# Kernel optimization log

Measured on AMD Instinct MI355X. Metric: run time of the kernel, lower is better.

## Reference

```python
import jax, jax.numpy as jnp
import numpy as np

# Model dims (see init_kwargs)
B, S, H = 1, 1024, 2048
NH, NKV, HD = 16, 4, 128       # query heads, kv heads (GQA), head dim
RD = 64                        # partial rotary dim
E, TOPK, I = 8, 2, 1024        # experts, top-k, expert intermediate
EPS = 1e-6
THETA = 1000000.0


def setup_inputs() -> dict:
    key = jax.random.key(0)
    ks = jax.random.split(key, 12)
    s = 0.02  # init scale
    return {
        "hidden_states": jax.random.normal(ks[0], (B, S, H), jnp.float32),
        "position_ids": jnp.tile(jnp.arange(S, dtype=jnp.int32), (B, 1)),
        "ln1_w": jnp.ones((H,), jnp.float32),
        "q_norm_w": jnp.ones((NH * HD,), jnp.float32),
        "k_norm_w": jnp.ones((NKV * HD,), jnp.float32),
        "wq": jax.random.normal(ks[1], (H, NH * HD), jnp.float32) * s,
        "wk": jax.random.normal(ks[2], (H, NKV * HD), jnp.float32) * s,
        "wv": jax.random.normal(ks[3], (H, NKV * HD), jnp.float32) * s,
        "wo": jax.random.normal(ks[4], (NH * HD, H), jnp.float32) * s,
        "ln2_w": jnp.ones((H,), jnp.float32),
        "router_w": jax.random.normal(ks[5], (H, E), jnp.float32) * s,
        "router_bias": jax.random.normal(ks[6], (E,), jnp.float32) * 0.1,
        "w_gate": jax.random.normal(ks[7], (E, H, I), jnp.float32) * s,
        "w_up": jax.random.normal(ks[8], (E, H, I), jnp.float32) * s,
        "w_down": jax.random.normal(ks[9], (E, I, H), jnp.float32) * s,
    }


def rmsnorm(x, w):
    # fp32 RMSNorm over full last dim (matches DistributedRMSNorm with tp=1)
    xf = x.astype(jnp.float32)
    r = jax.lax.rsqrt(jnp.mean(xf * xf, axis=-1, keepdims=True) + EPS)
    return (xf * r * w).astype(x.dtype)


def _rope(x, cos, sin):
    # partial rotary: only first RD dims of each head are rotated
    xr, xp = x[..., :RD], x[..., RD:]
    half = RD // 2
    rot = jnp.concatenate([-xr[..., half:], xr[..., :half]], axis=-1)
    return jnp.concatenate([xr * cos + rot * sin, xp], axis=-1)


def reference(hidden_states, position_ids, ln1_w, q_norm_w, k_norm_w,
              wq, wk, wv, wo, ln2_w, router_w, router_bias,
              w_gate, w_up, w_down):
    x = hidden_states
    # --- attention block ---
    h = rmsnorm(x, ln1_w)
    Q = h @ wq  # [B,S,NH*HD]
    K = h @ wk  # [B,S,NKV*HD]
    V = h @ wv
    # MiniMax M2 qk_norm: RMSNorm over FULL projection output BEFORE head reshape
    Q = rmsnorm(Q, q_norm_w)
    K = rmsnorm(K, k_norm_w)
    q = Q.reshape(B, S, NH, HD).transpose(0, 2, 1, 3)   # [B,NH,S,HD]
    k = K.reshape(B, S, NKV, HD).transpose(0, 2, 1, 3)  # [B,NKV,S,HD]
    v = V.reshape(B, S, NKV, HD).transpose(0, 2, 1, 3)
    # partial RoPE
    inv = 1.0 / (THETA ** (jnp.arange(0, RD, 2, dtype=jnp.float32) / RD))
    ang = position_ids.astype(jnp.float32)[:, :, None] * inv  # [B,S,RD/2]
    cos = jnp.concatenate([jnp.cos(ang)] * 2, axis=-1)[:, None]  # [B,1,S,RD]
    sin = jnp.concatenate([jnp.sin(ang)] * 2, axis=-1)[:, None]
    q = _rope(q, cos, sin)
    k = _rope(k, cos, sin)
    # GQA expand
    rep = NH // NKV
    k = jnp.repeat(k, rep, axis=1)
    v = jnp.repeat(v, rep, axis=1)
    scores = jnp.einsum('bhqd,bhkd->bhqk', q, k).astype(jnp.float32) / np.sqrt(HD).astype(np.float32)
    causal = jnp.tril(jnp.ones((S, S), bool))
    scores = jnp.where(causal, scores, jnp.float32(-1e30))
    attn = jax.nn.softmax(scores, axis=-1).astype(v.dtype)
    ctx = jnp.einsum('bhqk,bhkd->bhqd', attn, v)
    attn_out = ctx.transpose(0, 2, 1, 3).reshape(B, S, NH * HD) @ wo
    res = x + attn_out
    # --- MoE block ---
    h2 = rmsnorm(res, ln2_w)
    t = h2.reshape(B * S, H)
    logits = t.astype(jnp.float32) @ router_w        # [T,E]
    sc = jax.nn.sigmoid(logits)
    # top-k chosen on bias-corrected scores; weights from uncorrected scores
    _, ti = jax.lax.top_k(sc + router_bias, TOPK)    # [T,TOPK]
    aff = jnp.take_along_axis(sc, ti, axis=-1)
    aff = aff / jnp.sum(aff, axis=-1, keepdims=True)  # normalize_top_k_affinities
    T = B * S
    combine = jnp.zeros((T, E), jnp.float32).at[jnp.arange(T)[:, None], ti].add(aff)
    # SwiGLU experts (dense-compute, sparse-combine reference for blockwise grouped GEMM)
    g = jnp.einsum('th,ehi->tei', t, w_gate)
    u = jnp.einsum('th,ehi->tei', t, w_up)
    act = jax.nn.silu(g) * u
    eo = jnp.einsum('tei,eih->teh', act, w_down)
    moe = jnp.einsum('te,teh->th', combine.astype(eo.dtype), eo)
    return res + moe.reshape(B, S, H)
```

## Files before the change

kernel.cpp:

```cpp
#include <hip/hip_runtime.h>
#include <hip/hip_bf16.h>
#include <cstdint>

static constexpr int S   = 1024;
static constexpr int H   = 2048;
static constexpr int NH  = 16;
static constexpr int NKV = 4;
static constexpr int HD  = 128;
static constexpr int EXPN = 8;
static constexpr int FFI = 1024;

typedef __bf16 bf16x8 __attribute__((ext_vector_type(8)));
typedef float  f32x4  __attribute__((ext_vector_type(4)));
typedef unsigned short ushortx8 __attribute__((ext_vector_type(8)));
typedef unsigned short ushortx4 __attribute__((ext_vector_type(4)));

#define DEVI __device__ __forceinline__

DEVI unsigned short f2bf(float f) {
    union { float f; uint32_t u; } v; v.f = f;
    uint32_t r = (v.u + 0x7FFFu + ((v.u >> 16) & 1u)) >> 16;
    return (unsigned short)r;
}
DEVI float bf2f(unsigned short s) {
    union { uint32_t u; float f; } v; v.u = ((uint32_t)s) << 16; return v.f;
}

DEVI void atomAdd(float* p, float v) { unsafeAtomicAdd(p, v); }

DEVI void gll16(const unsigned short* g, unsigned short* l) {
    __builtin_amdgcn_global_load_lds(
        (const __attribute__((address_space(1))) unsigned int*)(g),
        (__attribute__((address_space(3))) unsigned int*)(l),
        16, 0, 0);
}

template<int N> DEVI void waitvm() {
    if constexpr (N == 0)      asm volatile("s_waitcnt vmcnt(0)" ::: "memory");
    else if constexpr (N == 2) asm volatile("s_waitcnt vmcnt(2)" ::: "memory");
    else if constexpr (N == 4) asm volatile("s_waitcnt vmcnt(4)" ::: "memory");
    else if constexpr (N == 6) asm volatile("s_waitcnt vmcnt(6)" ::: "memory");
    else static_assert(N == 0 || N == 2 || N == 4 || N == 6, "unsupported vmcnt");
}
DEVI void pipe_barrier() {
    __builtin_amdgcn_sched_barrier(0);
    __builtin_amdgcn_s_barrier();
    __builtin_amdgcn_sched_barrier(0);
}

__global__ __launch_bounds__(256) void transT(const float* __restrict__ in,
                                              unsigned short* __restrict__ outp,
                                              int R, int C)
{
    __shared__ unsigned short tl[64][72];
    int zb = blockIdx.z;
    in   += (size_t)zb * R * C;
    outp += (size_t)zb * R * C;
    int c0 = blockIdx.x * 64, r0 = blockIdx.y * 64;
    int t = threadIdx.x;
    int cq = (t & 15) * 4;
    int rr = t >> 4;
    #pragma unroll
    for (int p = 0; p < 4; ++p) {
        int row = rr + p * 16;
        float4 v = *(const float4*)&in[(size_t)(r0 + row) * C + c0 + cq];
        tl[cq + 0][row] = f2bf(v.x);
        tl[cq + 1][row] = f2bf(v.y);
        tl[cq + 2][row] = f2bf(v.z);
        tl[cq + 3][row] = f2bf(v.w);
    }
    __syncthreads();
    int r8 = (t & 7) * 8;
    int cc = t >> 3;
    #pragma unroll
    for (int p = 0; p < 2; ++p) {
        int col = cc + p * 32;
        ushortx8 v = *(const ushortx8*)&tl[col][r8];
        *(ushortx8*)&outp[(size_t)(c0 + col) * R + r0 + r8] = v;
    }
}

enum { CFG_PROJ3 = 0, CFG_WO = 1, CFG_SCORES = 2, CFG_PV = 3, CFG_GATEUP = 4, CFG_DOWN = 5 };

template<int CFG, int WM, int NI, bool PIPE>
__global__ __launch_bounds__(256, 2) void gemm_k(
    const unsigned short* __restrict__ A,
    const unsigned short* __restrict__ B0,
    const unsigned short* __restrict__ B1,
    const unsigned short* __restrict__ B2,
    float* __restrict__ C0,
    float* __restrict__ C1,
    float* __restrict__ C2,
    unsigned short* __restrict__ Cb,
    const float* __restrict__ X,
    const int* __restrict__ cnt,
    const int* __restrict__ tokList,
    int arg0)
{
    constexpr bool DUAL = (CFG == CFG_GATEUP);
    constexpr int BM = WM * 32;
    constexpr int BN = NI * 32;
    constexpr int ASZ = BM * 64;
    constexpr int BSZ = BN * 64;
    constexpr int NBUF = PIPE ? 3 : 2;
    constexpr int LD = WM + NI + (DUAL ? NI : 0);

    const int tid = threadIdx.x;
    const int m0 = blockIdx.y * BM;
    int n0 = blockIdx.x * BN;

    int M = S;
    int kbeg = 0, kend = 0, LDA = 0, LDBK = 0, LDC = 0;
    const unsigned short* Ap = A;
    const unsigned short* Bb = B0;
    const unsigned short* Bb2 = B1;
    const int* tlist = nullptr;
    float* Cout = C0;
    int head = 0, e = 0, hl = 0;

    if constexpr (CFG == CFG_PROJ3) {
        int xt = blockIdx.x;
        if (xt < 32)      { Bb = B0; Cout = C0; LDC = 2048; n0 = xt * 64; }
        else if (xt < 40) { Bb = B1; Cout = C1; LDC = 512;  n0 = (xt - 32) * 64; }
        else              { Bb = B2; Cout = C2; LDC = 512;  n0 = (xt - 40) * 64; }
        LDA = H; LDBK = H; kend = H;
    } else if constexpr (CFG == CFG_WO) {
        LDA = H; LDBK = H; LDC = H; kend = H;
    } else if constexpr (CFG == CFG_SCORES) {
        hl = blockIdx.z; head = arg0 + hl;
        if (n0 >= m0 + BM) return;
        Ap = A + (size_t)head * S * HD;
        Bb = B0 + (size_t)(head >> 2) * S * HD;
        kend = HD; LDA = HD; LDBK = HD;
    } else if constexpr (CFG == CFG_PV) {
        int z = blockIdx.z; hl = z >> 2; int ks = z & 3;
        head = arg0 + hl;
        int kcap = m0 + BM;
        kbeg = ks * 256;
        if (kbeg >= kcap) return;
        kend = (kbeg + 256 < kcap) ? kbeg + 256 : kcap;
        Ap = A + (size_t)hl * S * S;
        Bb = B0 + (size_t)(head >> 2) * HD * S;
        LDA = S; LDBK = S;
    } else if constexpr (CFG == CFG_GATEUP) {
        e = blockIdx.z;
        M = cnt[e]; if (m0 >= M) return;
        tlist = tokList + e * S;
        Bb  = B0 + (size_t)e * FFI * H;
        Bb2 = B1 + (size_t)e * FFI * H;
        kend = H; LDA = H; LDBK = H;
    } else {
        e = blockIdx.z;
        M = cnt[e]; if (m0 >= M) return;
        Ap = A + (size_t)e * S * FFI;
        Bb = B0 + (size_t)e * H * FFI;
        kend = FFI; LDA = FFI; LDBK = FFI;
    }

    __shared__ unsigned short As[NBUF * ASZ];
    __shared__ unsigned short Bs[NBUF * BSZ];
    __shared__ unsigned short Bs2[DUAL ? NBUF * BSZ : 8];

    const int lane = tid & 63, grp = lane >> 4, r16 = lane & 15;
    const int wid = tid >> 6, wr = wid >> 1, wc = wid & 1;
    const int wbase8 = (tid & 0xFFC0) * 8;

    size_t aoff[WM];
    #pragma unroll
    for (int c = 0; c < WM; ++c) {
        int chunk = c * 256 + tid;
        int row = chunk >> 3;
        int kcs = (chunk & 7) * 8;
        int grow = m0 + row;
        if constexpr (CFG == CFG_GATEUP) { int r2 = grow < M ? grow : M - 1; grow = tlist[r2]; }
        else if constexpr (CFG == CFG_DOWN) { grow = grow < M ? grow : M - 1; }
        aoff[c] = (size_t)grow * LDA + (kcs ^ ((row & 7) << 3));
    }
    size_t boff[NI];
    #pragma unroll
    for (int c = 0; c < NI; ++c) {
        int chunk = c * 256 + tid;
        int row = chunk >> 3;
        int kcs = (chunk & 7) * 8;
        boff[c] = (size_t)(n0 + row) * LDBK + (kcs ^ ((row & 7) << 3));
    }

    auto STAGE = [&](int buf, int k0) {
        #pragma unroll
        for (int c = 0; c < WM; ++c)
            gll16(Ap + aoff[c] + k0, &As[buf * ASZ + c * 2048 + wbase8]);
        #pragma unroll
        for (int c = 0; c < NI; ++c)
            gll16(Bb + boff[c] + k0, &Bs[buf * BSZ + c * 2048 + wbase8]);
        if constexpr (DUAL) {
            #pragma unroll
            for (int c = 0; c < NI; ++c)
                gll16(Bb2 + boff[c] + k0, &Bs2[buf * BSZ + c * 2048 + wbase8]);
        }
    };

    f32x4 acc[WM][NI] = {};
    f32x4 acc2[DUAL ? WM : 1][DUAL ? NI : 1] = {};

    auto COMPUTE = [&](int buf) {
        #pragma unroll
        for (int kk = 0; kk < 64; kk += 32) {
            bf16x8 af[WM], bfr[NI], bfr2[DUAL ? NI : 1];
            #pragma unroll
            for (int mi = 0; mi < WM; ++mi) {
                int r = wr * (WM * 16) + mi * 16 + r16;
                int idx = buf * ASZ + r * 64 + ((kk + grp * 8) ^ ((r & 7) << 3));
                af[mi] = __builtin_bit_cast(bf16x8, *(const ushortx8*)&As[idx]);
            }
            #pragma unroll
            for (int ni = 0; ni < NI; ++ni) {
                int r = wc * (NI * 16) + ni * 16 + r16;
                int idx = buf * BSZ + r * 64 + ((kk + grp * 8) ^ ((r & 7) << 3));
                bfr[ni] = __builtin_bit_cast(bf16x8, *(const ushortx8*)&Bs[idx]);
                if constexpr (DUAL)
                    bfr2[ni] = __builtin_bit_cast(bf16x8, *(const ushortx8*)&Bs2[idx]);
            }
            #pragma unroll
            for (int mi = 0; mi < WM; ++mi)
                #pragma unroll
                for (int ni = 0; ni < NI; ++ni) {
                    acc[mi][ni] = __builtin_amdgcn_mfma_f32_16x16x32_bf16(af[mi], bfr[ni], acc[mi][ni], 0, 0, 0);
                    if constexpr (DUAL)
                        acc2[mi][ni] = __builtin_amdgcn_mfma_f32_16x16x32_bf16(af[mi], bfr2[ni], acc2[mi][ni], 0, 0, 0);
                }
        }
    };

    if constexpr (PIPE) {
        const int nk = (kend - kbeg) >> 6;
        STAGE(0, kbeg);
        if (nk > 1) STAGE(1, kbeg + 64);
        if (nk > 1) waitvm<LD>(); else waitvm<0>();
        pipe_barrier();
        int cur = 0, stg = 2;
        for (int i = 0; i < nk; ++i) {
            if (i + 2 < nk) {
                STAGE(stg, kbeg + (i + 2) * 64);
                stg = (stg == 2) ? 0 : stg + 1;
            }
            COMPUTE(cur);
            cur = (cur == 2) ? 0 : cur + 1;
            if (i + 1 < nk) {
                if (i + 2 < nk) waitvm<LD>();
                else            waitvm<0>();
                pipe_barrier();
            }
        }
    } else {
        int cur = 0;
        STAGE(0, kbeg);
        __syncthreads();
        for (int k0 = kbeg; k0 < kend; k0 += 64) {
            if (k0 + 64 < kend) STAGE(cur ^ 1, k0 + 64);
            COMPUTE(cur);
            __syncthreads();
            cur ^= 1;
        }
    }

    #pragma unroll
    for (int mi = 0; mi < WM; ++mi) {
        #pragma unroll
        for (int ni = 0; ni < NI; ++ni) {
            f32x4 v = acc[mi][ni];
            int col = n0 + wc * (NI * 16) + ni * 16 + r16;
            #pragma unroll
            for (int j = 0; j < 4; ++j) {
                int row = m0 + wr * (WM * 16) + mi * 16 + grp * 4 + j;
                float val = v[j];
                if constexpr (CFG == CFG_PROJ3) {
                    Cout[(size_t)row * LDC + col] = val;
                } else if constexpr (CFG == CFG_WO) {
                    C0[(size_t)row * H + col] = val + X[(size_t)row * H + col];
                } else if constexpr (CFG == CFG_SCORES) {
                    float sv = val * 0.08838834764831845f;
                    if (col > row) sv = -1e30f;
                    Cb[((size_t)hl * S + row) * S + col] = f2bf(sv);
                } else if constexpr (CFG == CFG_PV) {
                    atomAdd(&C0[(size_t)row * 2048 + head * HD + col], val);
                } else if constexpr (CFG == CFG_GATEUP) {
                    if (row < M) {
                        float g = val, u = acc2[mi][ni][j];
                        float a = g / (1.f + expf(-g)) * u;
                        Cb[((size_t)e * S + row) * FFI + col] = f2bf(a);
                    }
                } else {
                    if (row < M) {
                        Cb[((size_t)e * S + row) * H + col] = f2bf(val);
                    }
                }
            }
        }
    }
}

__global__ __launch_bounds__(256) void rms_h(const float* __restrict__ x,
                                             const float* __restrict__ w,
                                             unsigned short* __restrict__ out)
{
    int row = blockIdx.x, tid = threadIdx.x;
    const float* xr = x + (size_t)row * H;
    float4 a = *(const float4*)&xr[tid * 8];
    float4 b = *(const float4*)&xr[tid * 8 + 4];
    float vals[8] = { a.x, a.y, a.z, a.w, b.x, b.y, b.z, b.w };
    float ss = 0;
    #pragma unroll
    for (int j = 0; j < 8; ++j) ss += vals[j] * vals[j];
    __shared__ float red[4];
    #pragma unroll
    for (int o = 32; o; o >>= 1) ss += __shfl_down(ss, o);
    if ((tid & 63) == 0) red[tid >> 6] = ss;
    __syncthreads();
    float tot = red[0] + red[1] + red[2] + red[3];
    float r = rsqrtf(tot * (1.f / H) + 1e-6f);
    ushortx8 ov;
    #pragma unroll
    for (int j = 0; j < 8; ++j) ov[j] = f2bf(vals[j] * r * w[tid * 8 + j]);
    *(ushortx8*)&out[(size_t)row * H + tid * 8] = ov;
}

__global__ __launch_bounds__(256) void qnorm_rope(const float* __restrict__ qbuf,
                                                  const float* __restrict__ qw,
                                                  const int* __restrict__ pos,
                                                  unsigned short* __restrict__ qatt)
{
    int tok = blockIdx.x, tid = threadIdx.x;
    __shared__ float sh[2048];
    __shared__ float red[4];
    const float* xr = qbuf + (size_t)tok * 2048;
    float4 a = *(const float4*)&xr[tid * 8];
    float4 b = *(const float4*)&xr[tid * 8 + 4];
    *(float4*)&sh[tid * 8] = a;
    *(float4*)&sh[tid * 8 + 4] = b;
    float ss = a.x*a.x + a.y*a.y + a.z*a.z + a.w*a.w + b.x*b.x + b.y*b.y + b.z*b.z + b.w*b.w;
    #pragma unroll
    for (int o = 32; o; o >>= 1) ss += __shfl_down(ss, o);
    if ((tid & 63) == 0) red[tid >> 6] = ss;
    __syncthreads();
    float tot = red[0] + red[1] + red[2] + red[3];
    float r = rsqrtf(tot * (1.f / 2048.f) + 1e-6f);
    float p = (float)pos[tok];
    #pragma unroll
    for (int j = 0; j < 8; ++j) {
        int idx = tid * 8 + j;
        int d = idx & 127, hh = idx >> 7;
        float v = sh[idx] * r * qw[idx];
        float o;
        if (d < 64) {
            int jj = d & 31;
            float ang = p * expf((float)jj * -0.43173470268f);
            float c = cosf(ang), sn = sinf(ang);
            if (d < 32) { float v2 = sh[idx + 32] * r * qw[idx + 32]; o = v * c - v2 * sn; }
            else        { float v2 = sh[idx - 32] * r * qw[idx - 32]; o = v * c + v2 * sn; }
        } else o = v;
        qatt[((size_t)hh * S + tok) * HD + d] = f2bf(o);
    }
}

__global__ __launch_bounds__(256) void knorm_rope(const float* __restrict__ kbuf,
                                                  const float* __restrict__ kw,
                                                  const int* __restrict__ pos,
                                                  unsigned short* __restrict__ katt)
{
    int tok = blockIdx.x, tid = threadIdx.x;
    __shared__ float sh[512];
    __shared__ float red[4];
    const float* xr = kbuf + (size_t)tok * 512;
    float2 a = *(const float2*)&xr[tid * 2];
    sh[tid * 2] = a.x; sh[tid * 2 + 1] = a.y;
    float ss = a.x * a.x + a.y * a.y;
    #pragma unroll
    for (int o = 32; o; o >>= 1) ss += __shfl_down(ss, o);
    if ((tid & 63) == 0) red[tid >> 6] = ss;
    __syncthreads();
    float tot = red[0] + red[1] + red[2] + red[3];
    float r = rsqrtf(tot * (1.f / 512.f) + 1e-6f);
    float p = (float)pos[tok];
    #pragma unroll
    for (int j = 0; j < 2; ++j) {
        int idx = tid * 2 + j;
        int d = idx & 127, hh = idx >> 7;
        float v = sh[idx] * r * kw[idx];
        float o;
        if (d < 64) {
            int jj = d & 31;
            float ang = p * expf((float)jj * -0.43173470268f);
            float c = cosf(ang), sn = sinf(ang);
            if (d < 32) { float v2 = sh[idx + 32] * r * kw[idx + 32]; o = v * c - v2 * sn; }
            else        { float v2 = sh[idx - 32] * r * kw[idx - 32]; o = v * c + v2 * sn; }
        } else o = v;
        katt[((size_t)hh * S + tok) * HD + d] = f2bf(o);
    }
}

__global__ __launch_bounds__(256) void softmax_k(unsigned short* __restrict__ sc)
{
    int bid = blockIdx.x;
    int hl = bid >> 10, q = bid & 1023;
    unsigned short* srow = sc + ((size_t)hl * S + q) * S;
    int L = q + 1, tid = threadIdx.x;
    __shared__ float red[4];
    ushortx4 in4 = *(const ushortx4*)&srow[tid * 4];
    float v[4]; float mx = -3.4e38f;
    #pragma unroll
    for (int i = 0; i < 4; ++i) {
        int j = tid * 4 + i;
        if (j < L) { v[i] = bf2f(in4[i]); mx = fmaxf(mx, v[i]); }
        else v[i] = -3.4e38f;
    }
    float m = mx;
    #pragma unroll
    for (int o = 32; o; o >>= 1) m = fmaxf(m, __shfl_down(m, o));
    if ((tid & 63) == 0) red[tid >> 6] = m;
    __syncthreads();
    float M_ = fmaxf(fmaxf(red[0], red[1]), fmaxf(red[2], red[3]));
    __syncthreads();
    float e[4]; float sum = 0;
    #pragma unroll
    for (int i = 0; i < 4; ++i) {
        int j = tid * 4 + i;
        if (j < L) { e[i] = expf(v[i] - M_); sum += e[i]; } else e[i] = 0.f;
    }
    #pragma unroll
    for (int o = 32; o; o >>= 1) sum += __shfl_down(sum, o);
    if ((tid & 63) == 0) red[tid >> 6] = sum;
    __syncthreads();
    float inv = 1.f / (red[0] + red[1] + red[2] + red[3]);
    ushortx4 o4;
    #pragma unroll
    for (int i = 0; i < 4; ++i) o4[i] = f2bf(e[i] * inv);
    *(ushortx4*)&srow[tid * 4] = o4;
}

__global__ void zero_cnt(int* cnt) { if (threadIdx.x < EXPN) cnt[threadIdx.x] = 0; }

__global__ void zerok(float4* __restrict__ p, int n4)
{
    int i = blockIdx.x * 256 + threadIdx.x;
    if (i < n4) p[i] = float4{0.f, 0.f, 0.f, 0.f};
}

__global__ void cvt_k(const float* __restrict__ src, unsigned short* __restrict__ dst)
{
    int i = blockIdx.x * 256 + threadIdx.x;
    float4 a = *(const float4*)&src[i * 8];
    float4 b = *(const float4*)&src[i * 8 + 4];
    float v[8] = { a.x, a.y, a.z, a.w, b.x, b.y, b.z, b.w };
    ushortx8 o;
    #pragma unroll
    for (int j = 0; j < 8; ++j) o[j] = f2bf(v[j]);
    *(ushortx8*)&dst[i * 8] = o;
}

__global__ __launch_bounds__(256) void router_k(const float* __restrict__ res,
                                                const float* __restrict__ ln2w,
                                                const float* __restrict__ rw,
                                                const float* __restrict__ rbias,
                                                int* __restrict__ cnt,
                                                int* __restrict__ tokList,
                                                int* __restrict__ slot,
                                                float* __restrict__ slotw)
{
    int tok = blockIdx.x, tid = threadIdx.x;
    const float* xr = res + (size_t)tok * H;
    float4 a = *(const float4*)&xr[tid * 8];
    float4 b = *(const float4*)&xr[tid * 8 + 4];
    float vals[8] = { a.x, a.y, a.z, a.w, b.x, b.y, b.z, b.w };
    float ss = 0;
    #pragma unroll
    for (int j = 0; j < 8; ++j) ss += vals[j] * vals[j];
    __shared__ float red[4];
    float t_ = ss;
    #pragma unroll
    for (int o = 32; o; o >>= 1) t_ += __shfl_down(t_, o);
    if ((tid & 63) == 0) red[tid >> 6] = t_;
    __syncthreads();
    float tot = red[0] + red[1] + red[2] + red[3];
    float r = rsqrtf(tot * (1.f / H) + 1e-6f);

    float acc[EXPN] = {};
    #pragma unroll
    for (int j = 0; j < 8; ++j) {
        float tv = vals[j] * r * ln2w[tid * 8 + j];
        const float* rp = rw + (size_t)(tid * 8 + j) * EXPN;
        #pragma unroll
        for (int e = 0; e < EXPN; ++e) acc[e] += tv * rp[e];
    }
    __shared__ float r8[4][EXPN];
    #pragma unroll
    for (int e = 0; e < EXPN; ++e) {
        float s_ = acc[e];
        #pragma unroll
        for (int o = 32; o; o >>= 1) s_ += __shfl_down(s_, o);
        acc[e] = s_;
    }
    if ((tid & 63) == 0)
        for (int e = 0; e < EXPN; ++e) r8[tid >> 6][e] = acc[e];
    __syncthreads();
    if (tid == 0) {
        float sg[EXPN];
        for (int e = 0; e < EXPN; ++e) {
            float lg = r8[0][e] + r8[1][e] + r8[2][e] + r8[3][e];
            sg[e] = 1.f / (1.f + expf(-lg));
        }
        int i0 = 0; float b0 = -1e30f;
        for (int e = 0; e < EXPN; ++e) {
            float s_ = sg[e] + rbias[e];
            if (s_ > b0) { b0 = s_; i0 = e; }
        }
        int i1 = -1; float b1 = -1e30f;
        for (int e = 0; e < EXPN; ++e) {
            if (e == i0) continue;
            float s_ = sg[e] + rbias[e];
            if (s_ > b1) { b1 = s_; i1 = e; }
        }
        float a0 = sg[i0], a1 = sg[i1], inv = 1.f / (a0 + a1);
        int p0 = atomicAdd(&cnt[i0], 1);
        tokList[i0 * S + p0] = tok;
        int p1 = atomicAdd(&cnt[i1], 1);
        tokList[i1 * S + p1] = tok;
        slot[tok * 2]     = i0 * S + p0;  slotw[tok * 2]     = a0 * inv;
        slot[tok * 2 + 1] = i1 * S + p1;  slotw[tok * 2 + 1] = a1 * inv;
    }
}

__global__ __launch_bounds__(256) void combine_k(const unsigned short* __restrict__ eo,
                                                 const int* __restrict__ slot,
                                                 const float* __restrict__ slotw,
                                                 float* __restrict__ out)
{
    int t = blockIdx.x;
    int c = threadIdx.x * 8;
    int s0 = slot[t * 2], s1 = slot[t * 2 + 1];
    float w0 = slotw[t * 2], w1 = slotw[t * 2 + 1];
    ushortx8 a = *(const ushortx8*)&eo[(size_t)s0 * H + c];
    ushortx8 b = *(const ushortx8*)&eo[(size_t)s1 * H + c];
    size_t base = (size_t)t * H + c;
    float4 o0 = *(float4*)&out[base];
    float4 o1 = *(float4*)&out[base + 4];
    float ov[8] = { o0.x, o0.y, o0.z, o0.w, o1.x, o1.y, o1.z, o1.w };
    #pragma unroll
    for (int j = 0; j < 8; ++j)
        ov[j] += w0 * bf2f(a[j]) + w1 * bf2f(b[j]);
    *(float4*)&out[base]     = float4{ ov[0], ov[1], ov[2], ov[3] };
    *(float4*)&out[base + 4] = float4{ ov[4], ov[5], ov[6], ov[7] };
}

extern "C" void kernel_launch(void* const* d_in, const int* in_sizes, int n_in,
                              void* d_out, int out_size, void* d_ws, size_t ws_size,
                              hipStream_t stream)
{
    const float* x     = (const float*)d_in[0];
    const int*   pos   = (const int*)d_in[1];
    const float* ln1w  = (const float*)d_in[2];
    const float* qnw   = (const float*)d_in[3];
    const float* knw   = (const float*)d_in[4];
    const float* wq    = (const float*)d_in[5];
    const float* wk    = (const float*)d_in[6];
    const float* wv    = (const float*)d_in[7];
    const float* wo    = (const float*)d_in[8];
    const float* ln2w  = (const float*)d_in[9];
    const float* rw    = (const float*)d_in[10];
    const float* rbias = (const float*)d_in[11];
    const float* wg    = (const float*)d_in[12];
    const float* wu    = (const float*)d_in[13];
    const float* wd    = (const float*)d_in[14];
    float* out = (float*)d_out;

    char* ws = (char*)d_ws;
    const size_t MB = 1024 * 1024;
    unsigned short* h_bf = (unsigned short*)(ws + 0);
    float* qbuf  = (float*)(ws + 4 * MB);
    float* ctxf  = (float*)(ws + 4 * MB);
    float* kbuf  = (float*)(ws + 12 * MB);
    float* vbuf  = (float*)(ws + 14 * MB);
    unsigned short* qatt = (unsigned short*)(ws + 16 * MB);
    unsigned short* katt = (unsigned short*)(ws + 20 * MB);
    unsigned short* vT   = (unsigned short*)(ws + 21 * MB);
    unsigned short* ctx  = (unsigned short*)(ws + 22 * MB);
    unsigned short* tbf  = (unsigned short*)(ws + 26 * MB);
    int*   cnt     = (int*)(ws + 30 * MB);
    int*   tokList = (int*)(ws + 30 * MB + 4096);
    int*   slot    = (int*)(ws + 30 * MB + 512 * 1024);
    float* slotw   = (float*)(ws + 30 * MB + 768 * 1024);
    unsigned short* scores = (unsigned short*)(ws + 31 * MB);
    unsigned short* act = (unsigned short*)(ws + 31 * MB);
    unsigned short* eo  = (unsigned short*)(ws + 47 * MB);
    unsigned short* wqT = (unsigned short*)(ws + 79 * MB);
    unsigned short* wkT = (unsigned short*)(ws + 87 * MB);
    unsigned short* wvT = (unsigned short*)(ws + 89 * MB);
    unsigned short* woT = (unsigned short*)(ws + 91 * MB);
    unsigned short* wgT = (unsigned short*)(ws + 99 * MB);
    unsigned short* wuT = (unsigned short*)(ws + 131 * MB);
    unsigned short* wdT = (unsigned short*)(ws + 163 * MB);

    transT<<<dim3(32, 32, 1), 256, 0, stream>>>(wq, wqT, 2048, 2048);
    transT<<<dim3(8,  32, 1), 256, 0, stream>>>(wk, wkT, 2048, 512);
    transT<<<dim3(8,  32, 1), 256, 0, stream>>>(wv, wvT, 2048, 512);
    transT<<<dim3(32, 32, 1), 256, 0, stream>>>(wo, woT, 2048, 2048);
    transT<<<dim3(16, 32, 8), 256, 0, stream>>>(wg, wgT, 2048, 1024);
    transT<<<dim3(16, 32, 8), 256, 0, stream>>>(wu, wuT, 2048, 1024);
    transT<<<dim3(32, 16, 8), 256, 0, stream>>>(wd, wdT, 1024, 2048);

    rms_h<<<S, 256, 0, stream>>>(x, ln1w, h_bf);

    gemm_k<CFG_PROJ3, 2, 2, true><<<dim3(48, 16, 1), 256, 0, stream>>>(h_bf, wqT, wkT, wvT, qbuf, kbuf, vbuf, nullptr, nullptr, nullptr, nullptr, 0);

    qnorm_rope<<<S, 256, 0, stream>>>(qbuf, qnw, pos, qatt);
    knorm_rope<<<S, 256, 0, stream>>>(kbuf, knw, pos, katt);
    transT<<<dim3(8, 16, 1), 256, 0, stream>>>(vbuf, vT, 1024, 512);
    zerok<<<2048, 256, 0, stream>>>((float4*)ctxf, (8 * MB) / 16);

    gemm_k<CFG_SCORES, 2, 4, false><<<dim3(8, 16, 16), 256, 0, stream>>>(qatt, katt, nullptr, nullptr, nullptr, nullptr, nullptr, scores, nullptr, nullptr, nullptr, 0);
    softmax_k<<<16 * S, 256, 0, stream>>>(scores);
    gemm_k<CFG_PV, 2, 2, true><<<dim3(2, 16, 64), 256, 0, stream>>>(scores, vT, nullptr, nullptr, ctxf, nullptr, nullptr, nullptr, nullptr, nullptr, nullptr, 0);
    cvt_k<<<(S * 2048) / (256 * 8), 256, 0, stream>>>(ctxf, ctx);

    gemm_k<CFG_WO, 2, 2, true><<<dim3(32, 16, 1), 256, 0, stream>>>(ctx, woT, nullptr, nullptr, out, nullptr, nullptr, nullptr, x, nullptr, nullptr, 0);

    rms_h<<<S, 256, 0, stream>>>(out, ln2w, tbf);
    zero_cnt<<<1, 64, 0, stream>>>(cnt);
    router_k<<<S, 256, 0, stream>>>(out, ln2w, rw, rbias, cnt, tokList, slot, slotw);

    gemm_k<CFG_GATEUP, 2, 1, true><<<dim3(32, 16, EXPN), 256, 0, stream>>>(tbf, wgT, wuT, nullptr, nullptr, nullptr, nullptr, act, nullptr, cnt, tokList, 0);
    gemm_k<CFG_DOWN, 2, 2, true><<<dim3(32, 16, EXPN), 256, 0, stream>>>(act, wdT, nullptr, nullptr, nullptr, nullptr, nullptr, eo, nullptr, cnt, tokList, 0);
    combine_k<<<S, 256, 0, stream>>>(eo, slot, slotw, out);
}
```

Before: 352.1 us.

## Concatenate gate/up weights into one GEMM and split SiLU into separate kernel

Measured after the change: 358.4 us. No clear change (+1.8%).

```diff
diff --git a/kernel.cpp b/kernel.cpp
--- a/kernel.cpp
+++ b/kernel.cpp
@@ -50,12 +50,13 @@
 
 __global__ __launch_bounds__(256) void transT(const float* __restrict__ in,
                                               unsigned short* __restrict__ outp,
-                                              int R, int C)
+                                              int R, int C,
+                                              size_t izs, size_t ozs)
 {
     __shared__ unsigned short tl[64][72];
     int zb = blockIdx.z;
-    in   += (size_t)zb * R * C;
-    outp += (size_t)zb * R * C;
+    in   += (size_t)zb * izs;
+    outp += (size_t)zb * ozs;
     int c0 = blockIdx.x * 64, r0 = blockIdx.y * 64;
     int t = threadIdx.x;
     int cq = (t & 15) * 4;
@@ -80,7 +81,7 @@
     }
 }
 
-enum { CFG_PROJ3 = 0, CFG_WO = 1, CFG_SCORES = 2, CFG_PV = 3, CFG_GATEUP = 4, CFG_DOWN = 5 };
+enum { CFG_PROJ3 = 0, CFG_WO = 1, CFG_SCORES = 2, CFG_PV = 3, CFG_GU = 4, CFG_DOWN = 5 };
 
 template<int CFG, int WM, int NI, bool PIPE>
 __global__ __launch_bounds__(256, 2) void gemm_k(
@@ -97,13 +98,12 @@
     const int* __restrict__ tokList,
     int arg0)
 {
-    constexpr bool DUAL = (CFG == CFG_GATEUP);
     constexpr int BM = WM * 32;
     constexpr int BN = NI * 32;
     constexpr int ASZ = BM * 64;
     constexpr int BSZ = BN * 64;
     constexpr int NBUF = PIPE ? 3 : 2;
-    constexpr int LD = WM + NI + (DUAL ? NI : 0);
+    constexpr int LD = WM + NI;
 
     const int tid = threadIdx.x;
     const int m0 = blockIdx.y * BM;
@@ -113,7 +113,6 @@
     int kbeg = 0, kend = 0, LDA = 0, LDBK = 0, LDC = 0;
     const unsigned short* Ap = A;
     const unsigned short* Bb = B0;
-    const unsigned short* Bb2 = B1;
     const int* tlist = nullptr;
     float* Cout = C0;
     int head = 0, e = 0, hl = 0;
@@ -142,12 +141,11 @@
         Ap = A + (size_t)hl * S * S;
         Bb = B0 + (size_t)(head >> 2) * HD * S;
         LDA = S; LDBK = S;
-    } else if constexpr (CFG == CFG_GATEUP) {
+    } else if constexpr (CFG == CFG_GU) {
         e = blockIdx.z;
         M = cnt[e]; if (m0 >= M) return;
         tlist = tokList + e * S;
-        Bb  = B0 + (size_t)e * FFI * H;
-        Bb2 = B1 + (size_t)e * FFI * H;
+        Bb = B0 + (size_t)e * 2048 * H;
         kend = H; LDA = H; LDBK = H;
     } else {
         e = blockIdx.z;
@@ -159,7 +157,6 @@
 
     __shared__ unsigned short As[NBUF * ASZ];
     __shared__ unsigned short Bs[NBUF * BSZ];
-    __shared__ unsigned short Bs2[DUAL ? NBUF * BSZ : 8];
 
     const int lane = tid & 63, grp = lane >> 4, r16 = lane & 15;
     const int wid = tid >> 6, wr = wid >> 1, wc = wid & 1;
@@ -172,7 +169,7 @@
         int row = chunk >> 3;
         int kcs = (chunk & 7) * 8;
         int grow = m0 + row;
-        if constexpr (CFG == CFG_GATEUP) { int r2 = grow < M ? grow : M - 1; grow = tlist[r2]; }
+        if constexpr (CFG == CFG_GU) { int r2 = grow < M ? grow : M - 1; grow = tlist[r2]; }
         else if constexpr (CFG == CFG_DOWN) { grow = grow < M ? grow : M - 1; }
         aoff[c] = (size_t)grow * LDA + (kcs ^ ((row & 7) << 3));
     }
@@ -192,20 +189,14 @@
         #pragma unroll
         for (int c = 0; c < NI; ++c)
             gll16(Bb + boff[c] + k0, &Bs[buf * BSZ + c * 2048 + wbase8]);
-        if constexpr (DUAL) {
-            #pragma unroll
-            for (int c = 0; c < NI; ++c)
-                gll16(Bb2 + boff[c] + k0, &Bs2[buf * BSZ + c * 2048 + wbase8]);
-        }
     };
 
     f32x4 acc[WM][NI] = {};
-    f32x4 acc2[DUAL ? WM : 1][DUAL ? NI : 1] = {};
 
     auto COMPUTE = [&](int buf) {
         #pragma unroll
         for (int kk = 0; kk < 64; kk += 32) {
-            bf16x8 af[WM], bfr[NI], bfr2[DUAL ? NI : 1];
+            bf16x8 af[WM], bfr[NI];
             #pragma unroll
             for (int mi = 0; mi < WM; ++mi) {
                 int r = wr * (WM * 16) + mi * 16 + r16;
@@ -217,17 +208,12 @@
                 int r = wc * (NI * 16) + ni * 16 + r16;
                 int idx = buf * BSZ + r * 64 + ((kk + grp * 8) ^ ((r & 7) << 3));
                 bfr[ni] = __builtin_bit_cast(bf16x8, *(const ushortx8*)&Bs[idx]);
-                if constexpr (DUAL)
-                    bfr2[ni] = __builtin_bit_cast(bf16x8, *(const ushortx8*)&Bs2[idx]);
             }
             #pragma unroll
             for (int mi = 0; mi < WM; ++mi)
                 #pragma unroll
-                for (int ni = 0; ni < NI; ++ni) {
+                for (int ni = 0; ni < NI; ++ni)
                     acc[mi][ni] = __builtin_amdgcn_mfma_f32_16x16x32_bf16(af[mi], bfr[ni], acc[mi][ni], 0, 0, 0);
-                    if constexpr (DUAL)
-                        acc2[mi][ni] = __builtin_amdgcn_mfma_f32_16x16x32_bf16(af[mi], bfr2[ni], acc2[mi][ni], 0, 0, 0);
-                }
         }
     };
 
@@ -283,11 +269,9 @@
                     Cb[((size_t)hl * S + row) * S + col] = f2bf(sv);
                 } else if constexpr (CFG == CFG_PV) {
                     atomAdd(&C0[(size_t)row * 2048 + head * HD + col], val);
-                } else if constexpr (CFG == CFG_GATEUP) {
+                } else if constexpr (CFG == CFG_GU) {
                     if (row < M) {
-                        float g = val, u = acc2[mi][ni][j];
-                        float a = g / (1.f + expf(-g)) * u;
-                        Cb[((size_t)e * S + row) * FFI + col] = f2bf(a);
+                        Cb[((size_t)e * S + row) * 2048 + col] = f2bf(val);
                     }
                 } else {
                     if (row < M) {
@@ -455,6 +439,25 @@
     #pragma unroll
     for (int j = 0; j < 8; ++j) o[j] = f2bf(v[j]);
     *(ushortx8*)&dst[i * 8] = o;
+}
+
+__global__ __launch_bounds__(256) void silu_k(const int* __restrict__ cnt,
+                                              const unsigned short* __restrict__ gu,
+                                              unsigned short* __restrict__ act)
+{
+    int e = blockIdx.y, row = blockIdx.x;
+    if (row >= cnt[e]) return;
+    size_t base = ((size_t)e * S + row) * 2048;
+    int i = threadIdx.x * 4;
+    ushortx4 g4 = *(const ushortx4*)&gu[base + i];
+    ushortx4 u4 = *(const ushortx4*)&gu[base + 1024 + i];
+    ushortx4 o4;
+    #pragma unroll
+    for (int j = 0; j < 4; ++j) {
+        float g = bf2f(g4[j]), u = bf2f(u4[j]);
+        o4[j] = f2bf(g / (1.f + expf(-g)) * u);
+    }
+    *(ushortx4*)&act[((size_t)e * S + row) * FFI + i] = o4;
 }
 
 __global__ __launch_bounds__(256) void router_k(const float* __restrict__ res,
@@ -589,23 +592,23 @@
     int*   slot    = (int*)(ws + 30 * MB + 512 * 1024);
     float* slotw   = (float*)(ws + 30 * MB + 768 * 1024);
     unsigned short* scores = (unsigned short*)(ws + 31 * MB);
-    unsigned short* act = (unsigned short*)(ws + 31 * MB);
-    unsigned short* eo  = (unsigned short*)(ws + 47 * MB);
-    unsigned short* wqT = (unsigned short*)(ws + 79 * MB);
-    unsigned short* wkT = (unsigned short*)(ws + 87 * MB);
-    unsigned short* wvT = (unsigned short*)(ws + 89 * MB);
-    unsigned short* woT = (unsigned short*)(ws + 91 * MB);
-    unsigned short* wgT = (unsigned short*)(ws + 99 * MB);
-    unsigned short* wuT = (unsigned short*)(ws + 131 * MB);
-    unsigned short* wdT = (unsigned short*)(ws + 163 * MB);
-
-    transT<<<dim3(32, 32, 1), 256, 0, stream>>>(wq, wqT, 2048, 2048);
-    transT<<<dim3(8,  32, 1), 256, 0, stream>>>(wk, wkT, 2048, 512);
-    transT<<<dim3(8,  32, 1), 256, 0, stream>>>(wv, wvT, 2048, 512);
-    transT<<<dim3(32, 32, 1), 256, 0, stream>>>(wo, woT, 2048, 2048);
-    transT<<<dim3(16, 32, 8), 256, 0, stream>>>(wg, wgT, 2048, 1024);
-    transT<<<dim3(16, 32, 8), 256, 0, stream>>>(wu, wuT, 2048, 1024);
-    transT<<<dim3(32, 16, 8), 256, 0, stream>>>(wd, wdT, 1024, 2048);
+    unsigned short* gu  = (unsigned short*)(ws + 31 * MB);
+    unsigned short* act = (unsigned short*)(ws + 63 * MB);
+    unsigned short* eo  = (unsigned short*)(ws + 31 * MB);
+    unsigned short* wqT  = (unsigned short*)(ws + 79 * MB);
+    unsigned short* wkT  = (unsigned short*)(ws + 87 * MB);
+    unsigned short* wvT  = (unsigned short*)(ws + 89 * MB);
+    unsigned short* woT  = (unsigned short*)(ws + 91 * MB);
+    unsigned short* wguT = (unsigned short*)(ws + 99 * MB);
+    unsigned short* wdT  = (unsigned short*)(ws + 163 * MB);
+
+    transT<<<dim3(32, 32, 1), 256, 0, stream>>>(wq, wqT, 2048, 2048, (size_t)2048 * 2048, (size_t)2048 * 2048);
+    transT<<<dim3(8,  32, 1), 256, 0, stream>>>(wk, wkT, 2048, 512, (size_t)2048 * 512, (size_t)2048 * 512);
+    transT<<<dim3(8,  32, 1), 256, 0, stream>>>(wv, wvT, 2048, 512, (size_t)2048 * 512, (size_t)2048 * 512);
+    transT<<<dim3(32, 32, 1), 256, 0, stream>>>(wo, woT, 2048, 2048, (size_t)2048 * 2048, (size_t)2048 * 2048);
+    transT<<<dim3(16, 32, 8), 256, 0, stream>>>(wg, wguT, 2048, 1024, (size_t)2048 * 1024, (size_t)2048 * 2048);
+    transT<<<dim3(16, 32, 8), 256, 0, stream>>>(wu, wguT + (size_t)1024 * 2048, 2048, 1024, (size_t)2048 * 1024, (size_t)2048 * 2048);
+    transT<<<dim3(32, 16, 8), 256, 0, stream>>>(wd, wdT, 1024, 2048, (size_t)1024 * 2048, (size_t)1024 * 2048);
 
     rms_h<<<S, 256, 0, stream>>>(x, ln1w, h_bf);
 
@@ -613,7 +616,7 @@
 
     qnorm_rope<<<S, 256, 0, stream>>>(qbuf, qnw, pos, qatt);
     knorm_rope<<<S, 256, 0, stream>>>(kbuf, knw, pos, katt);
-    transT<<<dim3(8, 16, 1), 256, 0, stream>>>(vbuf, vT, 1024, 512);
+    transT<<<dim3(8, 16, 1), 256, 0, stream>>>(vbuf, vT, 1024, 512, (size_t)1024 * 512, (size_t)1024 * 512);
     zerok<<<2048, 256, 0, stream>>>((float4*)ctxf, (8 * MB) / 16);
 
     gemm_k<CFG_SCORES, 2, 4, false><<<dim3(8, 16, 16), 256, 0, stream>>>(qatt, katt, nullptr, nullptr, nullptr, nullptr, nullptr, scores, nullptr, nullptr, nullptr, 0);
@@ -627,7 +630,8 @@
     zero_cnt<<<1, 64, 0, stream>>>(cnt);
     router_k<<<S, 256, 0, stream>>>(out, ln2w, rw, rbias, cnt, tokList, slot, slotw);
 
-    gemm_k<CFG_GATEUP, 2, 1, true><<<dim3(32, 16, EXPN), 256, 0, stream>>>(tbf, wgT, wuT, nullptr, nullptr, nullptr, nullptr, act, nullptr, cnt, tokList, 0);
+    gemm_k<CFG_GU, 2, 2, true><<<dim3(32, 16, EXPN), 256, 0, stream>>>(tbf, wguT, nullptr, nullptr, nullptr, nullptr, nullptr, gu, nullptr, cnt, tokList, 0);
+    silu_k<<<dim3(S, EXPN), 256, 0, stream>>>(cnt, gu, act);
     gemm_k<CFG_DOWN, 2, 2, true><<<dim3(32, 16, EXPN), 256, 0, stream>>>(act, wdT, nullptr, nullptr, nullptr, nullptr, nullptr, eo, nullptr, cnt, tokList, 0);
     combine_k<<<S, 256, 0, stream>>>(eo, slot, slotw, out);
 }
```
